# Kernel tuning notes

Hardware: AMD Instinct MI355X
Metric: run time of the kernel (lower is better)

The kernel has to match this reference:

```python
import jax, jax.numpy as jnp
import numpy as np

N_FEAT = 128
F_HID = 128


def setup_inputs() -> dict:
    key = jax.random.key(0)
    ks = jax.random.split(key, 9)
    N, E = 100000, 1600000
    x = jax.random.normal(ks[0], (N, N_FEAT), dtype=jnp.float32)
    edge_index = jax.random.randint(ks[1], (2, E), 0, N, dtype=jnp.int64)
    def glorot(k, fan_in, fan_out):
        lim = np.sqrt(6.0 / (fan_in + fan_out)).astype(np.float32)
        return jax.random.uniform(k, (fan_in, fan_out), jnp.float32, -lim, lim)
    return {
        "x": x,
        "edge_index": edge_index,
        "W1": glorot(ks[2], N_FEAT, F_HID), "b1": jnp.zeros((F_HID,), jnp.float32),
        "W2": glorot(ks[3], F_HID, F_HID), "b2": jnp.zeros((F_HID,), jnp.float32),
        "W3": glorot(ks[4], F_HID, F_HID), "b3": jnp.zeros((F_HID,), jnp.float32),
    }


def _gcn_conv(x, W, b, row, col, inv_sqrt_deg, n):
    # GCNConv: x' = D^{-1/2} (A + I) D^{-1/2} (x @ W) + b  (self-loops already in row/col)
    h = x @ W                                   # [N, F]
    norm = inv_sqrt_deg[row] * inv_sqrt_deg[col]  # [E']
    msg = h[col] * norm[:, None]                # gather + scale, [E', F]
    out = jax.ops.segment_sum(msg, row, num_segments=n)  # scatter-add, [N, F]
    return out + b


def reference(x, edge_index, W1, b1, W2, b2, W3, b3):
    n = x.shape[0]
    loops = jnp.arange(n, dtype=edge_index.dtype)
    row = jnp.concatenate([edge_index[0], loops])
    col = jnp.concatenate([edge_index[1], loops])
    deg = jax.ops.segment_sum(jnp.ones_like(row, dtype=x.dtype), row, num_segments=n)
    inv_sqrt_deg = jnp.where(deg > 0, jax.lax.rsqrt(jnp.maximum(deg, 1.0)), 0.0)
    h = _gcn_conv(x, W1, b1, row, col, inv_sqrt_deg, n)
    h = jax.nn.relu(h)  # dropout is identity in eval mode
    h = _gcn_conv(h, W2, b2, row, col, inv_sqrt_deg, n)
    h = jax.nn.relu(h)
    h = _gcn_conv(h, W3, b3, row, col, inv_sqrt_deg, n)
    return h
```

## Files before the change

kernel.cpp:

```cpp
#include <hip/hip_runtime.h>
#include <hip/hip_bf16.h>

#define NFEAT 128
#define EPB   4096
#define RPB   256
#define NBU_PAD 512
#define BCAP  6144

typedef short bf16x8 __attribute__((ext_vector_type(8)));
typedef float f32x4  __attribute__((ext_vector_type(4)));

__global__ __launch_bounds__(256) void a1_hist(const int* __restrict__ rows, int E,
                                               int* __restrict__ countsT, int nbu) {
    __shared__ int h[NBU_PAD];
    int t = threadIdx.x;
    for (int i = t; i < NBU_PAD; i += 256) h[i] = 0;
    __syncthreads();
    int e0 = blockIdx.x * EPB;
    int ecnt = min(EPB, E - e0);
    for (int k = t; k < ecnt; k += 256) atomicAdd(&h[rows[e0 + k] >> 8], 1);
    __syncthreads();
    for (int j = t; j < nbu; j += 256) countsT[(size_t)blockIdx.x * nbu + j] = h[j];
}

__global__ void transpose_counts(const int* __restrict__ in, int* __restrict__ out,
                                 int nbk, int nbu) {
    int i = blockIdx.x * 256 + threadIdx.x;
    if (i < nbk * nbu) {
        int b = i / nbk, blk = i - b * nbk;
        out[i] = in[(size_t)blk * nbu + b];
    }
}

#define SCAN_B 1024
__global__ void scanA_kernel(const int* __restrict__ in, int K,
                             int* __restrict__ excl, int* __restrict__ bsums) {
    __shared__ int sm[SCAN_B];
    int t = threadIdx.x;
    int g = blockIdx.x * SCAN_B + t;
    int v = (g < K) ? in[g] : 0;
    sm[t] = v;
    __syncthreads();
    for (int off = 1; off < SCAN_B; off <<= 1) {
        int u = (t >= off) ? sm[t - off] : 0;
        __syncthreads();
        sm[t] += u;
        __syncthreads();
    }
    if (g < K) excl[g] = sm[t] - v;
    if (t == SCAN_B - 1) bsums[blockIdx.x] = sm[t];
}

__global__ void scanB_kernel(int* __restrict__ bsums, int nb) {
    __shared__ int s[256];
    int t = threadIdx.x;
    int v = (t < nb) ? bsums[t] : 0;
    s[t] = v;
    __syncthreads();
    for (int off = 1; off < 256; off <<= 1) {
        int u = (t >= off) ? s[t - off] : 0;
        __syncthreads();
        s[t] += u;
        __syncthreads();
    }
    if (t < nb) bsums[t] = s[t] - v;
}

__global__ __launch_bounds__(256) void a2_scatter(const int* __restrict__ rows,
                                                  const int* __restrict__ colsIn, int E,
                                                  const int* __restrict__ scanArr,
                                                  const int* __restrict__ bsums,
                                                  int nbk, int nbu,
                                                  int* __restrict__ packed) {
    __shared__ int cnt[NBU_PAD], start[NBU_PAD], cur[NBU_PAD];
    __shared__ int sortedV[EPB];
    __shared__ unsigned short sortedB[EPB];
    __shared__ int p[256];
    int t = threadIdx.x, blk = blockIdx.x;
    for (int i = t; i < NBU_PAD; i += 256) cnt[i] = 0;
    __syncthreads();
    int e0 = blk * EPB;
    int ecnt = min(EPB, E - e0);
    int myr[16], myc[16];
#pragma unroll
    for (int k = 0; k < 16; ++k) {
        int idx = k * 256 + t;
        if (idx < ecnt) {
            myr[k] = rows[e0 + idx];
            myc[k] = colsIn[e0 + idx];
            atomicAdd(&cnt[myr[k] >> 8], 1);
        }
    }
    __syncthreads();
    int a0 = cnt[2 * t], a1 = cnt[2 * t + 1];
    p[t] = a0 + a1;
    __syncthreads();
    for (int off = 1; off < 256; off <<= 1) {
        int u = (t >= off) ? p[t - off] : 0;
        __syncthreads();
        p[t] += u;
        __syncthreads();
    }
    int ex = p[t] - (a0 + a1);
    start[2 * t] = ex;      start[2 * t + 1] = ex + a0;
    cur[2 * t] = ex;        cur[2 * t + 1] = ex + a0;
    __syncthreads();
#pragma unroll
    for (int k = 0; k < 16; ++k) {
        int idx = k * 256 + t;
        if (idx < ecnt) {
            int b = myr[k] >> 8;
            int pos = atomicAdd(&cur[b], 1);
            sortedV[pos] = ((myr[k] & 255) << 17) | myc[k];
            sortedB[pos] = (unsigned short)b;
        }
    }
    __syncthreads();
    for (int j = t; j < nbu; j += 256) {
        int idx = j * nbk + blk;
        cnt[j] = scanArr[idx] + bsums[idx >> 10] - start[j];
    }
    __syncthreads();
    for (int i = t; i < ecnt; i += 256) {
        int b = sortedB[i];
        packed[cnt[b] + i] = sortedV[i];
    }
}

__global__ __launch_bounds__(256) void b_sort(const int* __restrict__ packed,
                                              const int* __restrict__ scanArr,
                                              const int* __restrict__ bsums,
                                              int nbk, int nbu, int N, int E,
                                              int* __restrict__ colSort,
                                              int* __restrict__ row_ptr,
                                              float* __restrict__ inv) {
    __shared__ int cnt[RPB], start[RPB], cur[RPB], s[RPB];
    __shared__ int sv[BCAP];
    int t = threadIdx.x, b = blockIdx.x;
    int i0 = b * nbk;
    int base = scanArr[i0] + bsums[i0 >> 10];
    int nxt;
    if (b + 1 < nbu) {
        int i1 = (b + 1) * nbk;
        nxt = scanArr[i1] + bsums[i1 >> 10];
    } else nxt = E;
    int sz = nxt - base;
    cnt[t] = 0;
    __syncthreads();
    for (int i = t; i < sz; i += 256) atomicAdd(&cnt[(packed[base + i] >> 17) & 255], 1);
    __syncthreads();
    int c = cnt[t];
    s[t] = c;
    __syncthreads();
    for (int off = 1; off < 256; off <<= 1) {
        int u = (t >= off) ? s[t - off] : 0;
        __syncthreads();
        s[t] += u;
        __syncthreads();
    }
    start[t] = s[t] - c;
    cur[t] = s[t] - c;
    __syncthreads();
    for (int i = t; i < sz; i += 256) {
        int v = packed[base + i];
        int lr = (v >> 17) & 255;
        int pos = atomicAdd(&cur[lr], 1);
        if (pos < BCAP) sv[pos] = v & 0x1FFFF;
    }
    __syncthreads();
    for (int i = t; i < sz; i += 256) colSort[base + i] = sv[i] << 8;
    int r = b * RPB + t;
    if (r < N) {
        row_ptr[r] = base + start[t];
        inv[r] = rsqrtf((float)(c + 1));
    }
    if (b == 0 && t == 0) row_ptr[N] = E;
}

__device__ inline unsigned short f2bf(float x) {
    unsigned u = __float_as_uint(x);
    unsigned r = (u + 0x7FFFu + ((u >> 16) & 1u)) >> 16;
    return (unsigned short)r;
}

__device__ inline unsigned cvt_pk_bf16(float a, float b) {
    unsigned r;
    asm("v_cvt_pk_bf16_f32 %0, %1, %2" : "=v"(r) : "v"(a), "v"(b));
    return r;
}

__device__ inline void split2(float x0, float x1, unsigned& hw, unsigned& lw) {
    unsigned u0 = __float_as_uint(x0), u1 = __float_as_uint(x1);
    hw = (u1 & 0xFFFF0000u) | (u0 >> 16);
    float l0 = x0 - __uint_as_float(u0 & 0xFFFF0000u);
    float l1 = x1 - __uint_as_float(u1 & 0xFFFF0000u);
    lw = (__float_as_uint(l1) & 0xFFFF0000u) | (__float_as_uint(l0) >> 16);
}

__global__ void wsplit3_kernel(const float* __restrict__ W1, const float* __restrict__ W2,
                               const float* __restrict__ W3,
                               unsigned short* __restrict__ WtH,
                               unsigned short* __restrict__ WtL) {
    int w = blockIdx.y;
    const float* W = (w == 0) ? W1 : (w == 1) ? W2 : W3;
    int i = blockIdx.x * 256 + threadIdx.x;
    int c = i >> 7, k = i & 127;
    float wv = W[k * NFEAT + c];
    unsigned u = __float_as_uint(wv);
    unsigned hib = u & 0xFFFF0000u;
    float lo = wv - __uint_as_float(hib);
    WtH[w * NFEAT * NFEAT + i] = (unsigned short)(u >> 16);
    WtL[w * NFEAT * NFEAT + i] = (unsigned short)(__float_as_uint(lo) >> 16);
}

__global__ __launch_bounds__(256) void gemm_mfma_f32(const float* __restrict__ X,
                                                     const unsigned short* __restrict__ Wt_hi,
                                                     const unsigned short* __restrict__ Wt_lo,
                                                     const float* __restrict__ inv,
                                                     unsigned short* __restrict__ Hn, int n) {
    int tid = threadIdx.x;
    int wave = tid >> 6, lane = tid & 63;
    int lrow = lane & 15, kgrp = lane >> 4;
    int wcol0 = wave * 32;
    int rowbase = blockIdx.x * 64;

    bf16x8 wh[2][4], wl[2][4];
#pragma unroll
    for (int ct = 0; ct < 2; ++ct) {
        int col = wcol0 + ct * 16 + lrow;
        const unsigned short* ph = Wt_hi + (size_t)col * NFEAT + kgrp * 8;
        const unsigned short* pl = Wt_lo + (size_t)col * NFEAT + kgrp * 8;
#pragma unroll
        for (int ks = 0; ks < 4; ++ks) {
            wh[ct][ks] = *(const bf16x8*)(ph + ks * 32);
            wl[ct][ks] = *(const bf16x8*)(pl + ks * 32);
        }
    }

    union U8 { bf16x8 v; unsigned w[4]; };

#pragma unroll
    for (int rt = 0; rt < 4; ++rt) {
        int arow = rowbase + rt * 16 + lrow;
        int rc = arow < n ? arow : n - 1;
        const float* px = X + (size_t)rc * NFEAT + kgrp * 8;

        bf16x8 xh[4], xl[4];
#pragma unroll
        for (int ks = 0; ks < 4; ++ks) {
            float4 v0 = *(const float4*)(px + ks * 32);
            float4 v1 = *(const float4*)(px + ks * 32 + 4);
            U8 uh, ul;
            split2(v0.x, v0.y, uh.w[0], ul.w[0]);
            split2(v0.z, v0.w, uh.w[1], ul.w[1]);
            split2(v1.x, v1.y, uh.w[2], ul.w[2]);
            split2(v1.z, v1.w, uh.w[3], ul.w[3]);
            xh[ks] = uh.v;
            xl[ks] = ul.v;
        }

        f32x4 acc[2] = {{0.f, 0.f, 0.f, 0.f}, {0.f, 0.f, 0.f, 0.f}};
#pragma unroll
        for (int ks = 0; ks < 4; ++ks) {
#pragma unroll
            for (int ct = 0; ct < 2; ++ct) {
                acc[ct] = __builtin_amdgcn_mfma_f32_16x16x32_bf16(wh[ct][ks], xh[ks], acc[ct], 0, 0, 0);
                acc[ct] = __builtin_amdgcn_mfma_f32_16x16x32_bf16(wl[ct][ks], xh[ks], acc[ct], 0, 0, 0);
                acc[ct] = __builtin_amdgcn_mfma_f32_16x16x32_bf16(wh[ct][ks], xl[ks], acc[ct], 0, 0, 0);
            }
        }

        int xrow = rowbase + rt * 16 + lrow;
        if (xrow < n) {
            float sc = inv[xrow];
#pragma unroll
            for (int ct = 0; ct < 2; ++ct) {
                uint2 st;
                st.x = cvt_pk_bf16(acc[ct][0] * sc, acc[ct][1] * sc);
                st.y = cvt_pk_bf16(acc[ct][2] * sc, acc[ct][3] * sc);
                *(uint2*)(Hn + (size_t)xrow * NFEAT + wcol0 + ct * 16 + kgrp * 4) = st;
            }
        }
    }
}

__global__ __launch_bounds__(256) void gemm_mfma_bf16(const unsigned short* __restrict__ XH,
                                                      const unsigned short* __restrict__ XL,
                                                      const unsigned short* __restrict__ Wt_hi,
                                                      const unsigned short* __restrict__ Wt_lo,
                                                      const float* __restrict__ inv,
                                                      unsigned short* __restrict__ Hn, int n) {
    int tid = threadIdx.x;
    int wave = tid >> 6, lane = tid & 63;
    int lrow = lane & 15, kgrp = lane >> 4;
    int wcol0 = wave * 32;
    int rowbase = blockIdx.x * 64;

    bf16x8 wh[2][4], wl[2][4];
#pragma unroll
    for (int ct = 0; ct < 2; ++ct) {
        int col = wcol0 + ct * 16 + lrow;
        const unsigned short* ph = Wt_hi + (size_t)col * NFEAT + kgrp * 8;
        const unsigned short* pl = Wt_lo + (size_t)col * NFEAT + kgrp * 8;
#pragma unroll
        for (int ks = 0; ks < 4; ++ks) {
            wh[ct][ks] = *(const bf16x8*)(ph + ks * 32);
            wl[ct][ks] = *(const bf16x8*)(pl + ks * 32);
        }
    }

#pragma unroll
    for (int rt = 0; rt < 4; ++rt) {
        int arow = rowbase + rt * 16 + lrow;
        int rc = arow < n ? arow : n - 1;
        const unsigned short* pxh = XH + (size_t)rc * NFEAT + kgrp * 8;
        const unsigned short* pxl = XL + (size_t)rc * NFEAT + kgrp * 8;

        bf16x8 xh[4], xl[4];
#pragma unroll
        for (int ks = 0; ks < 4; ++ks) {
            xh[ks] = *(const bf16x8*)(pxh + ks * 32);
            xl[ks] = *(const bf16x8*)(pxl + ks * 32);
        }

        f32x4 acc[2] = {{0.f, 0.f, 0.f, 0.f}, {0.f, 0.f, 0.f, 0.f}};
#pragma unroll
        for (int ks = 0; ks < 4; ++ks) {
#pragma unroll
            for (int ct = 0; ct < 2; ++ct) {
                acc[ct] = __builtin_amdgcn_mfma_f32_16x16x32_bf16(wh[ct][ks], xh[ks], acc[ct], 0, 0, 0);
                acc[ct] = __builtin_amdgcn_mfma_f32_16x16x32_bf16(wl[ct][ks], xh[ks], acc[ct], 0, 0, 0);
                acc[ct] = __builtin_amdgcn_mfma_f32_16x16x32_bf16(wh[ct][ks], xl[ks], acc[ct], 0, 0, 0);
            }
        }

        int xrow = rowbase + rt * 16 + lrow;
        if (xrow < n) {
            float sc = inv[xrow];
#pragma unroll
            for (int ct = 0; ct < 2; ++ct) {
                uint2 st;
                st.x = cvt_pk_bf16(acc[ct][0] * sc, acc[ct][1] * sc);
                st.y = cvt_pk_bf16(acc[ct][2] * sc, acc[ct][3] * sc);
                *(uint2*)(Hn + (size_t)xrow * NFEAT + wcol0 + ct * 16 + kgrp * 4) = st;
            }
        }
    }
}

template <int RELU, int EMIT_SPLIT>
__global__ __launch_bounds__(256) void aggregate_bf16(const unsigned short* __restrict__ Hn,
                                                      const int* __restrict__ row_ptr,
                                                      const int* __restrict__ cols,
                                                      const float* __restrict__ inv,
                                                      const float* __restrict__ bias,
                                                      float* __restrict__ out,
                                                      unsigned short* __restrict__ XH,
                                                      unsigned short* __restrict__ XL, int n) {
    int node = blockIdx.x * (blockDim.x >> 6) + (threadIdx.x >> 6);
    if (node >= n) return;
    int lane = threadIdx.x & 63;
    int q = lane >> 4;
    unsigned fb = (lane & 15) << 4;
    const char* Hb = (const char*)Hn;

    float2 accA[4], accB[4];
#pragma unroll
    for (int k = 0; k < 4; ++k) {
        accA[k] = make_float2(0.f, 0.f);
        accB[k] = make_float2(0.f, 0.f);
    }

#define UNPK_ADD(ACC, W) do {                                              \
        unsigned _w = (W);                                                 \
        (ACC).x += __uint_as_float(_w << 16);                              \
        (ACC).y += __uint_as_float(_w & 0xFFFF0000u);                      \
    } while (0)

    if (q == 3) {
        uint4 v = *(const uint4*)(Hb + ((unsigned)node << 8) + fb);
        const unsigned* u = (const unsigned*)&v;
#pragma unroll
        for (int k = 0; k < 4; ++k) UNPK_ADD(accA[k], u[k]);
    }

    int s = row_ptr[node], e = row_ptr[node + 1];
    int j = s + q;
    for (; j + 12 < e; j += 16) {
        unsigned o0 = (unsigned)cols[j];
        unsigned o1 = (unsigned)cols[j + 4];
        unsigned o2 = (unsigned)cols[j + 8];
        unsigned o3 = (unsigned)cols[j + 12];
        uint4 v0 = *(const uint4*)(Hb + o0 + fb);
        uint4 v1 = *(const uint4*)(Hb + o1 + fb);
        uint4 v2 = *(const uint4*)(Hb + o2 + fb);
        uint4 v3 = *(const uint4*)(Hb + o3 + fb);
        const unsigned* u0 = (const unsigned*)&v0;
        const unsigned* u1 = (const unsigned*)&v1;
        const unsigned* u2 = (const unsigned*)&v2;
        const unsigned* u3 = (const unsigned*)&v3;
#pragma unroll
        for (int k = 0; k < 4; ++k) {
            UNPK_ADD(accA[k], u0[k]);
            UNPK_ADD(accB[k], u1[k]);
            UNPK_ADD(accA[k], u2[k]);
            UNPK_ADD(accB[k], u3[k]);
        }
    }
    for (; j + 4 < e; j += 8) {
        unsigned o0 = (unsigned)cols[j];
        unsigned o1 = (unsigned)cols[j + 4];
        uint4 v0 = *(const uint4*)(Hb + o0 + fb);
        uint4 v1 = *(const uint4*)(Hb + o1 + fb);
        const unsigned* u0 = (const unsigned*)&v0;
        const unsigned* u1 = (const unsigned*)&v1;
#pragma unroll
        for (int k = 0; k < 4; ++k) {
            UNPK_ADD(accA[k], u0[k]);
            UNPK_ADD(accB[k], u1[k]);
        }
    }
    if (j < e) {
        unsigned o0 = (unsigned)cols[j];
        uint4 v0 = *(const uint4*)(Hb + o0 + fb);
        const unsigned* u0 = (const unsigned*)&v0;
#pragma unroll
        for (int k = 0; k < 4; ++k) UNPK_ADD(accA[k], u0[k]);
    }
#undef UNPK_ADD

    float acc[8];
#pragma unroll
    for (int k = 0; k < 4; ++k) {
        acc[2 * k]     = accA[k].x + accB[k].x;
        acc[2 * k + 1] = accA[k].y + accB[k].y;
    }

#pragma unroll
    for (int k = 0; k < 8; ++k) {
        acc[k] += __shfl_xor(acc[k], 16, 64);
        acc[k] += __shfl_xor(acc[k], 32, 64);
    }

    if (q == 0) {
        unsigned f = (lane & 15) << 3;
        float inv_i = inv[node];
        float4 b0 = *(const float4*)(bias + f);
        float4 b1v = *(const float4*)(bias + f + 4);
        float r[8];
        r[0] = acc[0] * inv_i + b0.x; r[1] = acc[1] * inv_i + b0.y;
        r[2] = acc[2] * inv_i + b0.z; r[3] = acc[3] * inv_i + b0.w;
        r[4] = acc[4] * inv_i + b1v.x; r[5] = acc[5] * inv_i + b1v.y;
        r[6] = acc[6] * inv_i + b1v.z; r[7] = acc[7] * inv_i + b1v.w;
        if (RELU) {
#pragma unroll
            for (int k = 0; k < 8; ++k) r[k] = fmaxf(r[k], 0.f);
        }
        if (EMIT_SPLIT) {
            ushort4 hv[2], lv[2];
#pragma unroll
            for (int g = 0; g < 2; ++g) {
#pragma unroll
                for (int k = 0; k < 4; ++k) {
                    float y = r[g * 4 + k];
                    unsigned u = __float_as_uint(y);
                    unsigned short hb = (unsigned short)(u >> 16);
                    float lo = y - __uint_as_float(u & 0xFFFF0000u);
                    ((unsigned short*)&hv[g])[k] = hb;
                    ((unsigned short*)&lv[g])[k] = f2bf(lo);
                }
            }
            *(ushort4*)(XH + (size_t)node * NFEAT + f)     = hv[0];
            *(ushort4*)(XH + (size_t)node * NFEAT + f + 4) = hv[1];
            *(ushort4*)(XL + (size_t)node * NFEAT + f)     = lv[0];
            *(ushort4*)(XL + (size_t)node * NFEAT + f + 4) = lv[1];
        } else {
            *(float4*)(out + (size_t)node * NFEAT + f)     = make_float4(r[0], r[1], r[2], r[3]);
            *(float4*)(out + (size_t)node * NFEAT + f + 4) = make_float4(r[4], r[5], r[6], r[7]);
        }
    }
}

static inline size_t align256(size_t x) { return (x + 255) & ~(size_t)255; }

extern "C" void kernel_launch(void* const* d_in, const int* in_sizes, int n_in,
                              void* d_out, int out_size, void* d_ws, size_t ws_size,
                              hipStream_t stream) {
    const float* x   = (const float*)d_in[0];
    const int*   ei  = (const int*)d_in[1];
    const float* W1  = (const float*)d_in[2];
    const float* b1  = (const float*)d_in[3];
    const float* W2  = (const float*)d_in[4];
    const float* b2  = (const float*)d_in[5];
    const float* W3  = (const float*)d_in[6];
    const float* b3  = (const float*)d_in[7];
    float* out = (float*)d_out;

    const int N = in_sizes[0] / NFEAT;
    const int E = in_sizes[1] / 2;
    const int* rows = ei;
    const int* colsIn = ei + E;

    const int nbk = (E + EPB - 1) / EPB;
    const int nbu = (N + RPB - 1) / RPB;
    const int K = nbk * nbu;

    char* ws = (char*)d_ws;
    size_t off = 0;
    unsigned short* Hn = (unsigned short*)(ws + off);
    off = align256(off + (size_t)N * NFEAT * sizeof(unsigned short));
    unsigned short* XH = (unsigned short*)(ws + off);
    off = align256(off + (size_t)N * NFEAT * sizeof(unsigned short));
    unsigned short* XL = (unsigned short*)(ws + off);
    off = align256(off + (size_t)N * NFEAT * sizeof(unsigned short));
    int*   bufA    = (int*)(ws + off);   off = align256(off + (size_t)K * sizeof(int));
    int*   bufB    = (int*)(ws + off);   off = align256(off + (size_t)K * sizeof(int));
    int*   bsums   = (int*)(ws + off);   off = align256(off + (size_t)256 * sizeof(int));
    int*   packed  = (int*)(ws + off);   off = align256(off + (size_t)E * sizeof(int));
    int*   colSort = (int*)(ws + off);   off = align256(off + (size_t)E * sizeof(int));
    int*   row_ptr = (int*)(ws + off);   off = align256(off + (size_t)(N + 1) * sizeof(int));
    float* inv     = (float*)(ws + off); off = align256(off + (size_t)N * sizeof(float));
    unsigned short* WtH = (unsigned short*)(ws + off);
    off = align256(off + (size_t)3 * NFEAT * NFEAT * sizeof(unsigned short));
    unsigned short* WtL = (unsigned short*)(ws + off);
    off = align256(off + (size_t)3 * NFEAT * NFEAT * sizeof(unsigned short));
    (void)ws_size; (void)n_in; (void)out_size;

    const int nb2 = (K + SCAN_B - 1) / SCAN_B;

    wsplit3_kernel<<<dim3(64, 3), 256, 0, stream>>>(W1, W2, W3, WtH, WtL);

    a1_hist<<<nbk, 256, 0, stream>>>(rows, E, bufA, nbu);
    transpose_counts<<<(K + 255) / 256, 256, 0, stream>>>(bufA, bufB, nbk, nbu);
    scanA_kernel<<<nb2, SCAN_B, 0, stream>>>(bufB, K, bufA, bsums);
    scanB_kernel<<<1, 256, 0, stream>>>(bsums, nb2);
    a2_scatter<<<nbk, 256, 0, stream>>>(rows, colsIn, E, bufA, bsums, nbk, nbu, packed);
    b_sort<<<nbu, 256, 0, stream>>>(packed, bufA, bsums, nbk, nbu, N, E, colSort, row_ptr, inv);

    const int gemm_grid = (N + 63) / 64;
    const int agg_grid  = (N + 3) / 4;

    gemm_mfma_f32<<<gemm_grid, 256, 0, stream>>>(x, WtH, WtL, inv, Hn, N);
    aggregate_bf16<1, 1><<<agg_grid, 256, 0, stream>>>(Hn, row_ptr, colSort, inv, b1,
                                                       nullptr, XH, XL, N);
    gemm_mfma_bf16<<<gemm_grid, 256, 0, stream>>>(XH, XL, WtH + NFEAT * NFEAT, WtL + NFEAT * NFEAT,
                                                  inv, Hn, N);
    aggregate_bf16<1, 1><<<agg_grid, 256, 0, stream>>>(Hn, row_ptr, colSort, inv, b2,
                                                       nullptr, XH, XL, N);
    gemm_mfma_bf16<<<gemm_grid, 256, 0, stream>>>(XH, XL, WtH + 2 * NFEAT * NFEAT,
                                                  WtL + 2 * NFEAT * NFEAT, inv, Hn, N);
    aggregate_bf16<0, 0><<<agg_grid, 256, 0, stream>>>(Hn, row_ptr, colSort, inv, b3,
                                                       out, nullptr, nullptr, N);
}
```

Baseline: 373.8 us.

## Fuse CSR preprocessing kernels and overlap first GEMM with edge scatter

Merges the weight split, bucket histogram and a new global-atomic degree count into one launch, folds the count transpose into the scan kernel along with the inverse-sqrt-degree computation, and runs the layer-1 GEMM blocks in the same launch as the edge scatter. The degree is now computed early so the first GEMM no longer waits for the full CSR sort. This cuts kernel launches and lets independent work share the GPU. In exchange it adds an extra zeroing kernel and a pass of global atomics over all edges, and the mixed-role launches carry the shared-memory footprint of the scatter branch into the GEMM blocks, which may lower occupancy.

```diff
diff --git a/kernel.cpp b/kernel.cpp
--- a/kernel.cpp
+++ b/kernel.cpp
@@ -10,35 +10,89 @@
 typedef short bf16x8 __attribute__((ext_vector_type(8)));
 typedef float f32x4  __attribute__((ext_vector_type(4)));
 
-__global__ __launch_bounds__(256) void a1_hist(const int* __restrict__ rows, int E,
-                                               int* __restrict__ countsT, int nbu) {
-    __shared__ int h[NBU_PAD];
+__device__ inline unsigned short f2bf(float x) {
+    unsigned u = __float_as_uint(x);
+    unsigned r = (u + 0x7FFFu + ((u >> 16) & 1u)) >> 16;
+    return (unsigned short)r;
+}
+
+__device__ inline unsigned cvt_pk_bf16(float a, float b) {
+    unsigned r;
+    asm("v_cvt_pk_bf16_f32 %0, %1, %2" : "=v"(r) : "v"(a), "v"(b));
+    return r;
+}
+
+__device__ inline void split2(float x0, float x1, unsigned& hw, unsigned& lw) {
+    unsigned u0 = __float_as_uint(x0), u1 = __float_as_uint(x1);
+    hw = (u1 & 0xFFFF0000u) | (u0 >> 16);
+    float l0 = x0 - __uint_as_float(u0 & 0xFFFF0000u);
+    float l1 = x1 - __uint_as_float(u1 & 0xFFFF0000u);
+    lw = (__float_as_uint(l1) & 0xFFFF0000u) | (__float_as_uint(l0) >> 16);
+}
+
+__global__ void zero_deg(int* __restrict__ deg, int N) {
+    int i = blockIdx.x * 256 + threadIdx.x;
+    if (i < N) deg[i] = 0;
+}
+
+__global__ __launch_bounds__(256) void wsplit_hist_deg(const float* __restrict__ W1,
+                                                       const float* __restrict__ W2,
+                                                       const float* __restrict__ W3,
+                                                       unsigned short* __restrict__ WtH,
+                                                       unsigned short* __restrict__ WtL,
+                                                       const int* __restrict__ rows, int E,
+                                                       int* __restrict__ countsT, int nbu,
+                                                       int nbk, int* __restrict__ deg) {
     int t = threadIdx.x;
-    for (int i = t; i < NBU_PAD; i += 256) h[i] = 0;
-    __syncthreads();
-    int e0 = blockIdx.x * EPB;
+    if (blockIdx.x < 192) {
+        int w = blockIdx.x >> 6;
+        const float* W = (w == 0) ? W1 : (w == 1) ? W2 : W3;
+        int i = (blockIdx.x & 63) * 256 + t;
+        int c = i >> 7, k = i & 127;
+        float wv = W[k * NFEAT + c];
+        unsigned u = __float_as_uint(wv);
+        unsigned hib = u & 0xFFFF0000u;
+        float lo = wv - __uint_as_float(hib);
+        WtH[w * NFEAT * NFEAT + i] = (unsigned short)(u >> 16);
+        WtL[w * NFEAT * NFEAT + i] = (unsigned short)(__float_as_uint(lo) >> 16);
+        return;
+    }
+    if ((int)blockIdx.x < 192 + nbk) {
+        int blk = blockIdx.x - 192;
+        __shared__ int h[NBU_PAD];
+        for (int i = t; i < NBU_PAD; i += 256) h[i] = 0;
+        __syncthreads();
+        int e0 = blk * EPB;
+        int ecnt = min(EPB, E - e0);
+        for (int k = t; k < ecnt; k += 256) atomicAdd(&h[rows[e0 + k] >> 8], 1);
+        __syncthreads();
+        for (int j = t; j < nbu; j += 256) countsT[(size_t)blk * nbu + j] = h[j];
+        return;
+    }
+    int blk = blockIdx.x - 192 - nbk;
+    int e0 = blk * EPB;
     int ecnt = min(EPB, E - e0);
-    for (int k = t; k < ecnt; k += 256) atomicAdd(&h[rows[e0 + k] >> 8], 1);
-    __syncthreads();
-    for (int j = t; j < nbu; j += 256) countsT[(size_t)blockIdx.x * nbu + j] = h[j];
-}
-
-__global__ void transpose_counts(const int* __restrict__ in, int* __restrict__ out,
-                                 int nbk, int nbu) {
-    int i = blockIdx.x * 256 + threadIdx.x;
-    if (i < nbk * nbu) {
-        int b = i / nbk, blk = i - b * nbk;
-        out[i] = in[(size_t)blk * nbu + b];
-    }
+    for (int k = t; k < ecnt; k += 256) atomicAdd(&deg[rows[e0 + k]], 1);
 }
 
 #define SCAN_B 1024
-__global__ void scanA_kernel(const int* __restrict__ in, int K,
-                             int* __restrict__ excl, int* __restrict__ bsums) {
+__global__ void scanA_inv(const int* __restrict__ counts , int K,
+                          int nbk, int nbu, int nb2,
+                          int* __restrict__ excl, int* __restrict__ bsums,
+                          const int* __restrict__ deg, float* __restrict__ inv, int N) {
+    int t = threadIdx.x;
+    if ((int)blockIdx.x >= nb2) {
+        int i = ((int)blockIdx.x - nb2) * SCAN_B + t;
+        if (i < N) inv[i] = rsqrtf((float)(deg[i] + 1));
+        return;
+    }
     __shared__ int sm[SCAN_B];
-    int t = threadIdx.x;
     int g = blockIdx.x * SCAN_B + t;
-    int v = (g < K) ? in[g] : 0;
+    int v = 0;
+    if (g < K) {
+        int b = g / nbk, blk = g - b * nbk;
+        v = counts[(size_t)blk * nbu + b];
+    }
     sm[t] = v;
     __syncthreads();
     for (int off = 1; off < SCAN_B; off <<= 1) {
@@ -66,64 +120,133 @@
     if (t < nb) bsums[t] = s[t] - v;
 }
 
-__global__ __launch_bounds__(256) void a2_scatter(const int* __restrict__ rows,
-                                                  const int* __restrict__ colsIn, int E,
-                                                  const int* __restrict__ scanArr,
-                                                  const int* __restrict__ bsums,
-                                                  int nbk, int nbu,
-                                                  int* __restrict__ packed) {
-    __shared__ int cnt[NBU_PAD], start[NBU_PAD], cur[NBU_PAD];
-    __shared__ int sortedV[EPB];
-    __shared__ unsigned short sortedB[EPB];
-    __shared__ int p[256];
-    int t = threadIdx.x, blk = blockIdx.x;
-    for (int i = t; i < NBU_PAD; i += 256) cnt[i] = 0;
-    __syncthreads();
-    int e0 = blk * EPB;
-    int ecnt = min(EPB, E - e0);
-    int myr[16], myc[16];
-#pragma unroll
-    for (int k = 0; k < 16; ++k) {
-        int idx = k * 256 + t;
-        if (idx < ecnt) {
-            myr[k] = rows[e0 + idx];
-            myc[k] = colsIn[e0 + idx];
-            atomicAdd(&cnt[myr[k] >> 8], 1);
-        }
-    }
-    __syncthreads();
-    int a0 = cnt[2 * t], a1 = cnt[2 * t + 1];
-    p[t] = a0 + a1;
-    __syncthreads();
-    for (int off = 1; off < 256; off <<= 1) {
-        int u = (t >= off) ? p[t - off] : 0;
-        __syncthreads();
-        p[t] += u;
-        __syncthreads();
-    }
-    int ex = p[t] - (a0 + a1);
-    start[2 * t] = ex;      start[2 * t + 1] = ex + a0;
-    cur[2 * t] = ex;        cur[2 * t + 1] = ex + a0;
-    __syncthreads();
-#pragma unroll
-    for (int k = 0; k < 16; ++k) {
-        int idx = k * 256 + t;
-        if (idx < ecnt) {
-            int b = myr[k] >> 8;
-            int pos = atomicAdd(&cur[b], 1);
-            sortedV[pos] = ((myr[k] & 255) << 17) | myc[k];
-            sortedB[pos] = (unsigned short)b;
-        }
-    }
-    __syncthreads();
-    for (int j = t; j < nbu; j += 256) {
-        int idx = j * nbk + blk;
-        cnt[j] = scanArr[idx] + bsums[idx >> 10] - start[j];
-    }
-    __syncthreads();
-    for (int i = t; i < ecnt; i += 256) {
-        int b = sortedB[i];
-        packed[cnt[b] + i] = sortedV[i];
+__global__ __launch_bounds__(256) void a2_gemm1(
+        const int* __restrict__ rows, const int* __restrict__ colsIn, int E,
+        const int* __restrict__ scanArr, const int* __restrict__ bsums,
+        int nbk, int nbu, int* __restrict__ packed,
+        const float* __restrict__ X,
+        const unsigned short* __restrict__ Wt_hi, const unsigned short* __restrict__ Wt_lo,
+        const float* __restrict__ inv, unsigned short* __restrict__ Hn, int n) {
+    int t = threadIdx.x;
+    if ((int)blockIdx.x < nbk) {
+        __shared__ int cnt[NBU_PAD], start[NBU_PAD], cur[NBU_PAD];
+        __shared__ int sortedV[EPB];
+        __shared__ unsigned short sortedB[EPB];
+        __shared__ int p[256];
+        int blk = blockIdx.x;
+        for (int i = t; i < NBU_PAD; i += 256) cnt[i] = 0;
+        __syncthreads();
+        int e0 = blk * EPB;
+        int ecnt = min(EPB, E - e0);
+        int myr[16], myc[16];
+#pragma unroll
+        for (int k = 0; k < 16; ++k) {
+            int idx = k * 256 + t;
+            if (idx < ecnt) {
+                myr[k] = rows[e0 + idx];
+                myc[k] = colsIn[e0 + idx];
+                atomicAdd(&cnt[myr[k] >> 8], 1);
+            }
+        }
+        __syncthreads();
+        int a0 = cnt[2 * t], a1 = cnt[2 * t + 1];
+        p[t] = a0 + a1;
+        __syncthreads();
+        for (int off = 1; off < 256; off <<= 1) {
+            int u = (t >= off) ? p[t - off] : 0;
+            __syncthreads();
+            p[t] += u;
+            __syncthreads();
+        }
+        int ex = p[t] - (a0 + a1);
+        start[2 * t] = ex;      start[2 * t + 1] = ex + a0;
+        cur[2 * t] = ex;        cur[2 * t + 1] = ex + a0;
+        __syncthreads();
+#pragma unroll
+        for (int k = 0; k < 16; ++k) {
+            int idx = k * 256 + t;
+            if (idx < ecnt) {
+                int b = myr[k] >> 8;
+                int pos = atomicAdd(&cur[b], 1);
+                sortedV[pos] = ((myr[k] & 255) << 17) | myc[k];
+                sortedB[pos] = (unsigned short)b;
+            }
+        }
+        __syncthreads();
+        for (int j = t; j < nbu; j += 256) {
+            int idx = j * nbk + blk;
+            cnt[j] = scanArr[idx] + bsums[idx >> 10] - start[j];
+        }
+        __syncthreads();
+        for (int i = t; i < ecnt; i += 256) {
+            int b = sortedB[i];
+            packed[cnt[b] + i] = sortedV[i];
+        }
+        return;
+    }
+    int gblk = blockIdx.x - nbk;
+    int wave = t >> 6, lane = t & 63;
+    int lrow = lane & 15, kgrp = lane >> 4;
+    int wcol0 = wave * 32;
+    int rowbase = gblk * 64;
+
+    bf16x8 wh[2][4], wl[2][4];
+#pragma unroll
+    for (int ct = 0; ct < 2; ++ct) {
+        int col = wcol0 + ct * 16 + lrow;
+        const unsigned short* ph = Wt_hi + (size_t)col * NFEAT + kgrp * 8;
+        const unsigned short* pl = Wt_lo + (size_t)col * NFEAT + kgrp * 8;
+#pragma unroll
+        for (int ks = 0; ks < 4; ++ks) {
+            wh[ct][ks] = *(const bf16x8*)(ph + ks * 32);
+            wl[ct][ks] = *(const bf16x8*)(pl + ks * 32);
+        }
+    }
+
+    union U8 { bf16x8 v; unsigned w[4]; };
+
+#pragma unroll
+    for (int rt = 0; rt < 4; ++rt) {
+        int arow = rowbase + rt * 16 + lrow;
+        int rc = arow < n ? arow : n - 1;
+        const float* px = X + (size_t)rc * NFEAT + kgrp * 8;
+
+        bf16x8 xh[4], xl[4];
+#pragma unroll
+        for (int ks = 0; ks < 4; ++ks) {
+            float4 v0 = *(const float4*)(px + ks * 32);
+            float4 v1 = *(const float4*)(px + ks * 32 + 4);
+            U8 uh, ul;
+            split2(v0.x, v0.y, uh.w[0], ul.w[0]);
+            split2(v0.z, v0.w, uh.w[1], ul.w[1]);
+            split2(v1.x, v1.y, uh.w[2], ul.w[2]);
+            split2(v1.z, v1.w, uh.w[3], ul.w[3]);
+            xh[ks] = uh.v;
+            xl[ks] = ul.v;
+        }
+
+        f32x4 acc[2] = {{0.f, 0.f, 0.f, 0.f}, {0.f, 0.f, 0.f, 0.f}};
+#pragma unroll
+        for (int ks = 0; ks < 4; ++ks) {
+#pragma unroll
+            for (int ct = 0; ct < 2; ++ct) {
+                acc[ct] = __builtin_amdgcn_mfma_f32_16x16x32_bf16(wh[ct][ks], xh[ks], acc[ct], 0, 0, 0);
+                acc[ct] = __builtin_amdgcn_mfma_f32_16x16x32_bf16(wl[ct][ks], xh[ks], acc[ct], 0, 0, 0);
+                acc[ct] = __builtin_amdgcn_mfma_f32_16x16x32_bf16(wh[ct][ks], xl[ks], acc[ct], 0, 0, 0);
+            }
+        }
+
+        int xrow = rowbase + rt * 16 + lrow;
+        if (xrow < n) {
+            float sc = inv[xrow];
+#pragma unroll
+            for (int ct = 0; ct < 2; ++ct) {
+                uint2 st;
+                st.x = cvt_pk_bf16(acc[ct][0] * sc, acc[ct][1] * sc);
+                st.y = cvt_pk_bf16(acc[ct][2] * sc, acc[ct][3] * sc);
+                *(uint2*)(Hn + (size_t)xrow * NFEAT + wcol0 + ct * 16 + kgrp * 4) = st;
+            }
+        }
     }
 }
 
@@ -132,8 +255,7 @@
                                               const int* __restrict__ bsums,
                                               int nbk, int nbu, int N, int E,
                                               int* __restrict__ colSort,
-                                              int* __restrict__ row_ptr,
-                                              float* __restrict__ inv) {
+                                              int* __restrict__ row_ptr) {
     __shared__ int cnt[RPB], start[RPB], cur[RPB], s[RPB];
     __shared__ int sv[BCAP];
     int t = threadIdx.x, b = blockIdx.x;
@@ -170,118 +292,8 @@
     __syncthreads();
     for (int i = t; i < sz; i += 256) colSort[base + i] = sv[i] << 8;
     int r = b * RPB + t;
-    if (r < N) {
-        row_ptr[r] = base + start[t];
-        inv[r] = rsqrtf((float)(c + 1));
-    }
+    if (r < N) row_ptr[r] = base + start[t];
     if (b == 0 && t == 0) row_ptr[N] = E;
-}
-
-__device__ inline unsigned short f2bf(float x) {
-    unsigned u = __float_as_uint(x);
-    unsigned r = (u + 0x7FFFu + ((u >> 16) & 1u)) >> 16;
-    return (unsigned short)r;
-}
-
-__device__ inline unsigned cvt_pk_bf16(float a, float b) {
-    unsigned r;
-    asm("v_cvt_pk_bf16_f32 %0, %1, %2" : "=v"(r) : "v"(a), "v"(b));
-    return r;
-}
-
-__device__ inline void split2(float x0, float x1, unsigned& hw, unsigned& lw) {
-    unsigned u0 = __float_as_uint(x0), u1 = __float_as_uint(x1);
-    hw = (u1 & 0xFFFF0000u) | (u0 >> 16);
-    float l0 = x0 - __uint_as_float(u0 & 0xFFFF0000u);
-    float l1 = x1 - __uint_as_float(u1 & 0xFFFF0000u);
-    lw = (__float_as_uint(l1) & 0xFFFF0000u) | (__float_as_uint(l0) >> 16);
-}
-
-__global__ void wsplit3_kernel(const float* __restrict__ W1, const float* __restrict__ W2,
-                               const float* __restrict__ W3,
-                               unsigned short* __restrict__ WtH,
-                               unsigned short* __restrict__ WtL) {
-    int w = blockIdx.y;
-    const float* W = (w == 0) ? W1 : (w == 1) ? W2 : W3;
-    int i = blockIdx.x * 256 + threadIdx.x;
-    int c = i >> 7, k = i & 127;
-    float wv = W[k * NFEAT + c];
-    unsigned u = __float_as_uint(wv);
-    unsigned hib = u & 0xFFFF0000u;
-    float lo = wv - __uint_as_float(hib);
-    WtH[w * NFEAT * NFEAT + i] = (unsigned short)(u >> 16);
-    WtL[w * NFEAT * NFEAT + i] = (unsigned short)(__float_as_uint(lo) >> 16);
-}
-
-__global__ __launch_bounds__(256) void gemm_mfma_f32(const float* __restrict__ X,
-                                                     const unsigned short* __restrict__ Wt_hi,
-                                                     const unsigned short* __restrict__ Wt_lo,
-                                                     const float* __restrict__ inv,
-                                                     unsigned short* __restrict__ Hn, int n) {
-    int tid = threadIdx.x;
-    int wave = tid >> 6, lane = tid & 63;
-    int lrow = lane & 15, kgrp = lane >> 4;
-    int wcol0 = wave * 32;
-    int rowbase = blockIdx.x * 64;
-
-    bf16x8 wh[2][4], wl[2][4];
-#pragma unroll
-    for (int ct = 0; ct < 2; ++ct) {
-        int col = wcol0 + ct * 16 + lrow;
-        const unsigned short* ph = Wt_hi + (size_t)col * NFEAT + kgrp * 8;
-        const unsigned short* pl = Wt_lo + (size_t)col * NFEAT + kgrp * 8;
-#pragma unroll
-        for (int ks = 0; ks < 4; ++ks) {
-            wh[ct][ks] = *(const bf16x8*)(ph + ks * 32);
-            wl[ct][ks] = *(const bf16x8*)(pl + ks * 32);
-        }
-    }
-
-    union U8 { bf16x8 v; unsigned w[4]; };
-
-#pragma unroll
-    for (int rt = 0; rt < 4; ++rt) {
-        int arow = rowbase + rt * 16 + lrow;
-        int rc = arow < n ? arow : n - 1;
-        const float* px = X + (size_t)rc * NFEAT + kgrp * 8;
-
-        bf16x8 xh[4], xl[4];
-#pragma unroll
-        for (int ks = 0; ks < 4; ++ks) {
-            float4 v0 = *(const float4*)(px + ks * 32);
-            float4 v1 = *(const float4*)(px + ks * 32 + 4);
-            U8 uh, ul;
-            split2(v0.x, v0.y, uh.w[0], ul.w[0]);
-            split2(v0.z, v0.w, uh.w[1], ul.w[1]);
-            split2(v1.x, v1.y, uh.w[2], ul.w[2]);
-            split2(v1.z, v1.w, uh.w[3], ul.w[3]);
-            xh[ks] = uh.v;
-            xl[ks] = ul.v;
-        }
-
-        f32x4 acc[2] = {{0.f, 0.f, 0.f, 0.f}, {0.f, 0.f, 0.f, 0.f}};
-#pragma unroll
-        for (int ks = 0; ks < 4; ++ks) {
-#pragma unroll
-            for (int ct = 0; ct < 2; ++ct) {
-                acc[ct] = __builtin_amdgcn_mfma_f32_16x16x32_bf16(wh[ct][ks], xh[ks], acc[ct], 0, 0, 0);
-                acc[ct] = __builtin_amdgcn_mfma_f32_16x16x32_bf16(wl[ct][ks], xh[ks], acc[ct], 0, 0, 0);
-                acc[ct] = __builtin_amdgcn_mfma_f32_16x16x32_bf16(wh[ct][ks], xl[ks], acc[ct], 0, 0, 0);
-            }
-        }
-
-        int xrow = rowbase + rt * 16 + lrow;
-        if (xrow < n) {
-            float sc = inv[xrow];
-#pragma unroll
-            for (int ct = 0; ct < 2; ++ct) {
-                uint2 st;
-                st.x = cvt_pk_bf16(acc[ct][0] * sc, acc[ct][1] * sc);
-                st.y = cvt_pk_bf16(acc[ct][2] * sc, acc[ct][3] * sc);
-                *(uint2*)(Hn + (size_t)xrow * NFEAT + wcol0 + ct * 16 + kgrp * 4) = st;
-            }
-        }
-    }
 }
 
 __global__ __launch_bounds__(256) void gemm_mfma_bf16(const unsigned short* __restrict__ XH,
@@ -520,6 +532,7 @@
     int*   colSort = (int*)(ws + off);   off = align256(off + (size_t)E * sizeof(int));
     int*   row_ptr = (int*)(ws + off);   off = align256(off + (size_t)(N + 1) * sizeof(int));
     float* inv     = (float*)(ws + off); off = align256(off + (size_t)N * sizeof(float));
+    int*   deg     = (int*)(ws + off);   off = align256(off + (size_t)N * sizeof(int));
     unsigned short* WtH = (unsigned short*)(ws + off);
     off = align256(off + (size_t)3 * NFEAT * NFEAT * sizeof(unsigned short));
     unsigned short* WtL = (unsigned short*)(ws + off);
@@ -527,20 +540,20 @@
     (void)ws_size; (void)n_in; (void)out_size;
 
     const int nb2 = (K + SCAN_B - 1) / SCAN_B;
-
-    wsplit3_kernel<<<dim3(64, 3), 256, 0, stream>>>(W1, W2, W3, WtH, WtL);
-
-    a1_hist<<<nbk, 256, 0, stream>>>(rows, E, bufA, nbu);
-    transpose_counts<<<(K + 255) / 256, 256, 0, stream>>>(bufA, bufB, nbk, nbu);
-    scanA_kernel<<<nb2, SCAN_B, 0, stream>>>(bufB, K, bufA, bsums);
-    scanB_kernel<<<1, 256, 0, stream>>>(bsums, nb2);
-    a2_scatter<<<nbk, 256, 0, stream>>>(rows, colsIn, E, bufA, bsums, nbk, nbu, packed);
-    b_sort<<<nbu, 256, 0, stream>>>(packed, bufA, bsums, nbk, nbu, N, E, colSort, row_ptr, inv);
-
+    const int invb = (N + SCAN_B - 1) / SCAN_B;
     const int gemm_grid = (N + 63) / 64;
     const int agg_grid  = (N + 3) / 4;
 
-    gemm_mfma_f32<<<gemm_grid, 256, 0, stream>>>(x, WtH, WtL, inv, Hn, N);
+    zero_deg<<<(N + 255) / 256, 256, 0, stream>>>(deg, N);
+    wsplit_hist_deg<<<192 + 2 * nbk, 256, 0, stream>>>(W1, W2, W3, WtH, WtL,
+                                                       rows, E, bufA, nbu, nbk, deg);
+    scanA_inv<<<nb2 + invb, SCAN_B, 0, stream>>>(bufA, K, nbk, nbu, nb2, bufB, bsums,
+                                                 deg, inv, N);
+    scanB_kernel<<<1, 256, 0, stream>>>(bsums, nb2);
+    a2_gemm1<<<nbk + gemm_grid, 256, 0, stream>>>(rows, colsIn, E, bufB, bsums, nbk, nbu, packed,
+                                                  x, WtH, WtL, inv, Hn, N);
+    b_sort<<<nbu, 256, 0, stream>>>(packed, bufB, bsums, nbk, nbu, N, E, colSort, row_ptr);
+
     aggregate_bf16<1, 1><<<agg_grid, 256, 0, stream>>>(Hn, row_ptr, colSort, inv, b1,
                                                        nullptr, XH, XL, N);
     gemm_mfma_bf16<<<gemm_grid, 256, 0, stream>>>(XH, XL, WtH + NFEAT * NFEAT, WtL + NFEAT * NFEAT,
```

New measurement: 422.8 us. 13.1% more time.
